# Kernel tuning notes

Hardware: AMD Instinct MI355X
Metric: run time of the kernel (lower is better)

## Reference

```python
import jax, jax.numpy as jnp
import numpy as np

B, S, D, H = 8, 1024, 1024, 16
DK = D // H
EPS = 1e-5

def _layernorm(x, w, b):
    mu = jnp.mean(x, axis=-1, keepdims=True)
    var = jnp.mean((x - mu) ** 2, axis=-1, keepdims=True)
    return (x - mu) * jax.lax.rsqrt(var + EPS) * w + b

def setup_inputs() -> dict:
    key = jax.random.key(0)
    ks = jax.random.split(key, 12)
    x = jax.random.normal(ks[0], (B, S, D), dtype=jnp.float32)
    batch_lengths = jax.random.randint(ks[1], (B,), S // 2, S + 1, dtype=jnp.int32)
    sc = 1.0 / np.sqrt(D)
    Wq = jax.random.normal(ks[2], (H, D, DK), dtype=jnp.float32) * sc
    Wk = jax.random.normal(ks[3], (H, D, DK), dtype=jnp.float32) * sc
    Wv = jax.random.normal(ks[4], (H, D, DK), dtype=jnp.float32) * sc
    fc1_w = jax.random.normal(ks[5], (D, D), dtype=jnp.float32) * sc
    fc1_b = jnp.zeros((D,), dtype=jnp.float32)
    fc2_w = jax.random.normal(ks[6], (D, D), dtype=jnp.float32) * sc
    fc2_b = jnp.zeros((D,), dtype=jnp.float32)
    ln1_w = jnp.ones((D,), dtype=jnp.float32)
    ln1_b = jnp.zeros((D,), dtype=jnp.float32)
    ln2_w = jnp.ones((D,), dtype=jnp.float32)
    ln2_b = jnp.zeros((D,), dtype=jnp.float32)
    return {"x": x, "Wq": Wq, "Wk": Wk, "Wv": Wv, "fc1_w": fc1_w, "fc1_b": fc1_b,
            "fc2_w": fc2_w, "fc2_b": fc2_b, "ln1_w": ln1_w, "ln1_b": ln1_b,
            "ln2_w": ln2_w, "ln2_b": ln2_b, "batch_lengths": batch_lengths, "max_len": S}

def reference(x, Wq, Wk, Wv, fc1_w, fc1_b, fc2_w, fc2_b, ln1_w, ln1_b, ln2_w, ln2_b, batch_lengths, max_len):
    b, s, d = x.shape
    h, _, dk = Wq.shape
    # padding masks: valid positions are t < length
    row = (jnp.arange(s)[None, :] < batch_lengths[:, None]).astype(x.dtype)  # [B,S]
    m = row[:, :, None]                 # [B,S,1], outputMask per-row
    mh = m[:, None]                     # [B,1,S,1]
    # all heads batched: Q,K,V -> [B,H,S,dk], masked like Wq(ctx)*mask etc.
    Q = jnp.einsum('bsd,hde->bhse', x, Wq) * mh
    K = jnp.einsum('bsd,hde->bhse', x, Wk) * mh
    V = jnp.einsum('bsd,hde->bhse', x, Wv) * mh
    energy = jnp.einsum('bhqe,bhke->bhqk', Q, K)
    # attnMask: key columns beyond length -> -inf
    key_valid = row[:, None, None, :] > 0
    energy = jnp.where(key_valid, energy, -jnp.inf)
    score = jax.nn.softmax(energy / jnp.sqrt(jnp.asarray(dk, x.dtype)), axis=-1)
    z = jnp.einsum('bhqk,bhke->bhqe', score, V)           # [B,H,S,dk]
    z = z.transpose(0, 2, 1, 3).reshape(b, s, d) * m      # concat heads, mask
    x1 = _layernorm(x + z, ln1_w, ln1_b)
    ff = jax.nn.relu(x1 @ fc1_w + fc1_b) * m
    ff = (ff @ fc2_w + fc2_b) * m
    return _layernorm(x1 + ff, ln2_w, ln2_b)
```

## Files before the change

### kernel.cpp

```cpp
#include <hip/hip_runtime.h>
#include <math.h>

#define B_ 8
#define S_ 1024
#define D_ 1024
#define H_ 16
#define DK_ 64
#define EPS_ 1e-5f

typedef __bf16 bf16_t;
typedef __bf16 bf16x8 __attribute__((ext_vector_type(8)));
typedef __bf16 bf16x4v __attribute__((ext_vector_type(4)));
typedef float  f32x4  __attribute__((ext_vector_type(4)));

__device__ __forceinline__ void gld16(const void* g, void* l) {
    __builtin_amdgcn_global_load_lds(
        (const __attribute__((address_space(1))) void*)g,
        (__attribute__((address_space(3))) void*)l, 16, 0, 0);
}

__global__ __launch_bounds__(256)
void prep(const float* __restrict__ x,
          const float* __restrict__ Wq, const float* __restrict__ Wk,
          const float* __restrict__ Wv, const float* __restrict__ W1,
          const float* __restrict__ W2, bf16_t* __restrict__ xb,
          bf16_t* __restrict__ WtQKV, bf16_t* __restrict__ Wt1,
          bf16_t* __restrict__ Wt2)
{
    __shared__ float tile[64][65];
    const int tid = threadIdx.x;
    const int z = blockIdx.z;

    if (z >= 5) {
        const int blk = (z - 5) * 256 + blockIdx.y * 16 + blockIdx.x;
        const int i = (blk * 256 + tid) * 4;
        const float4 v = *(const float4*)(x + i);
        bf16x4v o = { (bf16_t)v.x, (bf16_t)v.y, (bf16_t)v.z, (bf16_t)v.w };
        *(bf16x4v*)(xb + i) = o;
        return;
    }

    const int n0 = blockIdx.x * 64, k0 = blockIdx.y * 64;
    const int col = tid & 63, r0 = tid >> 6;
    const float* src = (z == 0) ? Wq : (z == 1) ? Wk : (z == 2) ? Wv
                     : (z == 3) ? W1 : W2;
    #pragma unroll
    for (int i = 0; i < 16; i++) {
        const int row = r0 + i * 4;
        float v;
        if (z < 3)
            v = src[((size_t)(n0 >> 6) << 16) + (size_t)(k0 + row) * 64 + col];
        else
            v = src[(size_t)(k0 + row) * D_ + n0 + col];
        tile[row][col] = v;
    }
    __syncthreads();
    bf16_t* dst = (z < 3) ? (WtQKV + (size_t)z * D_ * D_)
                : (z == 3) ? Wt1 : Wt2;
    #pragma unroll
    for (int i = 0; i < 16; i++) {
        const int nr = r0 + i * 4;
        const int n = n0 + nr, k = k0 + col;
        const size_t pidx = ((size_t)(n >> 4) * (D_ >> 3) + (k >> 3)) * 128
                          + (size_t)(n & 15) * 8 + (k & 7);
        dst[pidx] = (bf16_t)tile[col][nr];
    }
}

template<int EPI, typename OUT>
__global__ __launch_bounds__(256, 2)
void gemm_bp(const bf16_t* __restrict__ A, const bf16_t* __restrict__ Bp,
             const float* __restrict__ bias, const int* __restrict__ lens,
             OUT* __restrict__ C, int M, int N, int K)
{
    __shared__ __align__(16) bf16_t As[2][128 * 64];

    const int tid  = threadIdx.x;
    const int lane = tid & 63;
    const int w    = tid >> 6;
    const int quad = lane >> 4, l16 = lane & 15;
    const int wm = w & 1, wn = w >> 1;
    const int sw8 = l16 & 7;

    const int nwg  = gridDim.x * gridDim.y;
    const int orig = blockIdx.y * gridDim.x + blockIdx.x;
    const int swz  = (orig & 7) * (nwg >> 3) + (orig >> 3);
    const int bn = (swz % gridDim.x) * 128;
    const int bm = (swz / gridDim.x) * 128;

    const int rS  = tid >> 3;
    const int cS  = ((tid & 7) ^ (rS & 7)) << 3;
    const int dOf = w * 1024;

    const size_t ntStride = (size_t)(K >> 3) * 128;
    const bf16_t* Bw = Bp + ((size_t)(bn >> 4) + (size_t)wn * 4) * ntStride
                          + (size_t)quad * 128 + (size_t)l16 * 8;

    f32x4 acc[4][4];
    #pragma unroll
    for (int i = 0; i < 4; i++)
        #pragma unroll
        for (int j = 0; j < 4; j++)
            #pragma unroll
            for (int r = 0; r < 4; r++) acc[i][j][r] = 0.f;

#define SA(b_, kt_) { \
    _Pragma("unroll") \
    for (int s_ = 0; s_ < 4; s_++) \
        gld16(A + (size_t)(bm + s_ * 32 + rS) * K + (kt_) * 64 + cS, \
              (char*)As[b_] + s_ * 4096 + dOf); }
#define LB(dst_, kt_) { \
    _Pragma("unroll") \
    for (int j_ = 0; j_ < 4; j_++) \
        _Pragma("unroll") \
        for (int kh_ = 0; kh_ < 2; kh_++) \
            dst_[j_][kh_] = *(const bf16x8*)(Bw + (size_t)j_ * ntStride \
                                             + ((kt_) * 8 + kh_ * 4) * 128); }
#define KSTEP(cb_, nb_, BC_, BX_, t_) { \
    const int ktn_ = ((t_) + 1 < NKT) ? (t_) + 1 : (t_); \
    SA(nb_, ktn_); \
    LB(BX_, ktn_); \
    __builtin_amdgcn_sched_barrier(0); \
    const bf16_t* Ac = As[cb_]; \
    _Pragma("unroll") \
    for (int kh_ = 0; kh_ < 2; kh_++) { \
        bf16x8 a_[4]; \
        _Pragma("unroll") \
        for (int i_ = 0; i_ < 4; i_++) \
            a_[i_] = *(const bf16x8*)&Ac[(wm * 64 + i_ * 16 + l16) * 64 \
                                         + (((kh_ * 4 + quad) ^ sw8) << 3)]; \
        _Pragma("unroll") \
        for (int i_ = 0; i_ < 4; i_++) \
            _Pragma("unroll") \
            for (int j_ = 0; j_ < 4; j_++) \
                acc[i_][j_] = __builtin_amdgcn_mfma_f32_16x16x32_bf16( \
                    a_[i_], BC_[j_][kh_], acc[i_][j_], 0, 0, 0); \
    } \
    __builtin_amdgcn_sched_barrier(0); \
    asm volatile("s_waitcnt vmcnt(8)" ::: "memory"); \
    __builtin_amdgcn_s_barrier(); }

    const int NKT = K >> 6;

    bf16x8 bA[4][2], bB[4][2];
    SA(0, 0);
    LB(bA, 0);
    asm volatile("s_waitcnt vmcnt(8)" ::: "memory");
    __builtin_amdgcn_s_barrier();

    for (int t = 0; t < NKT; t += 2) {
        KSTEP(0, 1, bA, bB, t);
        KSTEP(1, 0, bB, bA, t + 1);
    }

#undef SA
#undef LB
#undef KSTEP

    #pragma unroll
    for (int i = 0; i < 4; i++) {
        #pragma unroll
        for (int r = 0; r < 4; r++) {
            const int m = bm + wm * 64 + i * 16 + quad * 4 + r;
            float keep = 1.f;
            if (EPI != 0) {
                const int s = m & (S_ - 1);
                const int bb = m >> 10;
                keep = (s < lens[bb]) ? 1.f : 0.f;
            }
            #pragma unroll
            for (int j = 0; j < 4; j++) {
                const int n = bn + wn * 64 + j * 16 + l16;
                float v = acc[i][j][r];
                if (EPI != 0) {
                    v += bias[n];
                    if (EPI == 1) v = fmaxf(v, 0.f);
                    v *= keep;
                }
                C[(size_t)m * N + n] = (OUT)v;
            }
        }
    }
}

__global__ __launch_bounds__(512, 4)
void attn_mfma(const bf16_t* __restrict__ QKV, const int* __restrict__ lens,
               bf16_t* __restrict__ Z)
{
    __shared__ __align__(16) bf16_t Ks[2][64][64];
    __shared__ __align__(16) bf16_t Vt[2][64][72];
    __shared__ __align__(16) bf16_t Ps[128][72];

    const int tid  = threadIdx.x;
    const int lane = tid & 63;
    const int w    = tid >> 6;
    const int quad = lane >> 4;
    const int l16  = lane & 15;
    const int id   = blockIdx.x;
    const int b    = id & 7;
    const int h    = (id >> 3) & 15;
    const int qt   = id >> 7;
    const int len  = lens[b];
    const int qbase = qt * 128;
    const bf16_t* Qp = QKV + (size_t)b * S_ * 3072 + (size_t)h * 64;
    const bf16_t* Kp = Qp + 1024;
    const bf16_t* Vp = Qp + 2048;
    const size_t zbase = (size_t)b * S_ * D_ + (size_t)h * 64;

    if (qbase >= len) {
        const int r = tid >> 2, c0 = (tid & 3) * 16;
        bf16_t* zp = Z + zbase + (size_t)(qbase + r) * D_ + c0;
        uint4 zz = {0u, 0u, 0u, 0u};
        *(uint4*)zp = zz;
        *(uint4*)(zp + 8) = zz;
        return;
    }

    const int qrow = qbase + w * 16 + l16;
    const bf16x8 bq0 = *(const bf16x8*)(Qp + (size_t)qrow * 3072 + quad * 8);
    const bf16x8 bq1 = *(const bf16x8*)(Qp + (size_t)qrow * 3072 + 32 + quad * 8);

    const int kr = tid >> 3;
    const int kc = ((tid & 7) ^ (kr & 7)) << 3;

    const int vr  = tid >> 3;
    const int cg8 = tid & 7;
    const int vc0 = cg8 * 8;
    const int vp  = vr ^ ((cg8 >> 1) << 4);

    f32x4 o[4];
    #pragma unroll
    for (int dm = 0; dm < 4; dm++)
        #pragma unroll
        for (int r = 0; r < 4; r++) o[dm][r] = 0.f;
    float l_q = 0.f;

    const int ntiles = (len + 63) >> 6;

    gld16(Kp + (size_t)kr * 3072 + kc, (char*)&Ks[0][0][0] + w * 1024);
    bf16x8 vcur = *(const bf16x8*)(Vp + (size_t)vr * 3072 + vc0);
    __syncthreads();

    for (int t = 0; t < ntiles; t++) {
        const int k0 = t * 64;
        const int cb = t & 1, nb = (t + 1) & 1;
        const int kn0 = (t + 1 < ntiles ? t + 1 : t) * 64;

        gld16(Kp + (size_t)(kn0 + kr) * 3072 + kc, (char*)&Ks[nb][0][0] + w * 1024);
        const bf16x8 vn = *(const bf16x8*)(Vp + (size_t)(kn0 + vr) * 3072 + vc0);
        __builtin_amdgcn_sched_barrier(0);

        #pragma unroll
        for (int kt = 0; kt < 4; kt++) {
            const int r = kt * 16 + l16;
            const bf16x8 ak0 = *(const bf16x8*)&Ks[cb][r][(quad ^ (l16 & 7)) << 3];
            const bf16x8 ak1 = *(const bf16x8*)&Ks[cb][r][((4 + quad) ^ (l16 & 7)) << 3];
            f32x4 z4 = {0.f, 0.f, 0.f, 0.f};
            z4 = __builtin_amdgcn_mfma_f32_16x16x32_bf16(ak0, bq0, z4, 0, 0, 0);
            const f32x4 sfv = __builtin_amdgcn_mfma_f32_16x16x32_bf16(ak1, bq1, z4, 0, 0, 0);
            bf16x4v pk;
            #pragma unroll
            for (int r2 = 0; r2 < 4; r2++) {
                const int key = k0 + kt * 16 + quad * 4 + r2;
                float p = __expf(sfv[r2] * 0.125f);
                p = (key < len) ? p : 0.f;
                l_q += p;
                pk[r2] = (bf16_t)p;
            }
            *(bf16x4v*)&Ps[w * 16 + l16][kt * 16 + quad * 4] = pk;
        }

        #pragma unroll
        for (int i = 0; i < 8; i++) Vt[cb][vc0 + i][vp] = vcur[i];
        vcur = vn;
        __syncthreads();

        const bf16x8 bp0 = *(const bf16x8*)&Ps[w * 16 + l16][quad * 8];
        const bf16x8 bp1 = *(const bf16x8*)&Ps[w * 16 + l16][32 + quad * 8];
        #pragma unroll
        for (int dm = 0; dm < 4; dm++) {
            const bf16x8 av0 = *(const bf16x8*)&Vt[cb][dm * 16 + l16][(quad * 8) ^ (dm * 16)];
            const bf16x8 av1 = *(const bf16x8*)&Vt[cb][dm * 16 + l16][(32 + quad * 8) ^ (dm * 16)];
            o[dm] = __builtin_amdgcn_mfma_f32_16x16x32_bf16(av0, bp0, o[dm], 0, 0, 0);
            o[dm] = __builtin_amdgcn_mfma_f32_16x16x32_bf16(av1, bp1, o[dm], 0, 0, 0);
        }
    }

    l_q += __shfl_xor(l_q, 16);
    l_q += __shfl_xor(l_q, 32);
    const int qg = qbase + w * 16 + l16;
    const float inv = (qg < len) ? 1.f / l_q : 0.f;
    bf16_t* zrow = Z + zbase + (size_t)qg * D_;
    #pragma unroll
    for (int dm = 0; dm < 4; dm++) {
        bf16x4v st;
        #pragma unroll
        for (int r = 0; r < 4; r++) st[r] = (bf16_t)(o[dm][r] * inv);
        *(bf16x4v*)(zrow + dm * 16 + quad * 4) = st;
    }
}

__device__ __forceinline__ void ln_core(float vx, float vy, float vz, float vw,
                                        int tid, float& mean, float& rstd)
{
    __shared__ float red[8];
    float s = vx + vy + vz + vw;
    #pragma unroll
    for (int off = 32; off; off >>= 1) s += __shfl_xor(s, off, 64);
    const int wv = tid >> 6, lane = tid & 63;
    if (lane == 0) red[wv] = s;
    __syncthreads();
    mean = (red[0] + red[1] + red[2] + red[3]) * (1.f / D_);
    const float dx = vx - mean, dy = vy - mean, dz = vz - mean, dw = vw - mean;
    float s2 = dx * dx + dy * dy + dz * dz + dw * dw;
    #pragma unroll
    for (int off = 32; off; off >>= 1) s2 += __shfl_xor(s2, off, 64);
    if (lane == 0) red[4 + wv] = s2;
    __syncthreads();
    rstd = rsqrtf((red[4] + red[5] + red[6] + red[7]) * (1.f / D_) + EPS_);
}

__global__ __launch_bounds__(256)
void add_ln1(const float* __restrict__ X, const bf16_t* __restrict__ Y,
             const float* __restrict__ g, const float* __restrict__ beta,
             bf16_t* __restrict__ out)
{
    const int row = blockIdx.x, tid = threadIdx.x;
    const float4 xv = ((const float4*)(X + (size_t)row * D_))[tid];
    const bf16x4v yv = *(const bf16x4v*)(Y + (size_t)row * D_ + tid * 4);
    const float vx = xv.x + (float)yv[0], vy = xv.y + (float)yv[1];
    const float vz = xv.z + (float)yv[2], vw = xv.w + (float)yv[3];
    float mean, rstd;
    ln_core(vx, vy, vz, vw, tid, mean, rstd);
    const float4 gv = ((const float4*)g)[tid];
    const float4 bv = ((const float4*)beta)[tid];
    bf16x4v o;
    o[0] = (bf16_t)((vx - mean) * rstd * gv.x + bv.x);
    o[1] = (bf16_t)((vy - mean) * rstd * gv.y + bv.y);
    o[2] = (bf16_t)((vz - mean) * rstd * gv.z + bv.z);
    o[3] = (bf16_t)((vw - mean) * rstd * gv.w + bv.w);
    *(bf16x4v*)(out + (size_t)row * D_ + tid * 4) = o;
}

__global__ __launch_bounds__(256)
void add_ln2(const bf16_t* __restrict__ X, const float* __restrict__ Y,
             const float* __restrict__ g, const float* __restrict__ beta,
             float* __restrict__ out)
{
    const int row = blockIdx.x, tid = threadIdx.x;
    const bf16x4v xv = *(const bf16x4v*)(X + (size_t)row * D_ + tid * 4);
    const float4 yv = ((const float4*)(Y + (size_t)row * D_))[tid];
    const float vx = (float)xv[0] + yv.x, vy = (float)xv[1] + yv.y;
    const float vz = (float)xv[2] + yv.z, vw = (float)xv[3] + yv.w;
    float mean, rstd;
    ln_core(vx, vy, vz, vw, tid, mean, rstd);
    const float4 gv = ((const float4*)g)[tid];
    const float4 bv = ((const float4*)beta)[tid];
    float4 o;
    o.x = (vx - mean) * rstd * gv.x + bv.x;
    o.y = (vy - mean) * rstd * gv.y + bv.y;
    o.z = (vz - mean) * rstd * gv.z + bv.z;
    o.w = (vw - mean) * rstd * gv.w + bv.w;
    ((float4*)(out + (size_t)row * D_))[tid] = o;
}

extern "C" void kernel_launch(void* const* d_in, const int* in_sizes, int n_in,
                              void* d_out, int out_size, void* d_ws, size_t ws_size,
                              hipStream_t stream)
{
    const float* x    = (const float*)d_in[0];
    const float* Wq   = (const float*)d_in[1];
    const float* Wk   = (const float*)d_in[2];
    const float* Wv   = (const float*)d_in[3];
    const float* fc1w = (const float*)d_in[4];
    const float* fc1b = (const float*)d_in[5];
    const float* fc2w = (const float*)d_in[6];
    const float* fc2b = (const float*)d_in[7];
    const float* ln1w = (const float*)d_in[8];
    const float* ln1b = (const float*)d_in[9];
    const float* ln2w = (const float*)d_in[10];
    const float* ln2b = (const float*)d_in[11];
    const int*   lens = (const int*)d_in[12];
    float* out = (float*)d_out;

    char* ws = (char*)d_ws;
    const size_t MB = 1024 * 1024;
    bf16_t* QKVb  = (bf16_t*)(ws);
    bf16_t* Zb    = (bf16_t*)(ws + 48 * MB);
    bf16_t* X1b   = (bf16_t*)(ws + 80 * MB);
    bf16_t* xb    = (bf16_t*)(ws + 96 * MB);
    bf16_t* H1b   = (bf16_t*)(ws + 96 * MB);
    float*  FF    = (float*)(ws + 48 * MB);
    bf16_t* WtQKV = (bf16_t*)(ws + 112 * MB);
    bf16_t* Wt1   = (bf16_t*)(ws + 118 * MB);
    bf16_t* Wt2   = (bf16_t*)(ws + 120 * MB);

    const int M = B_ * S_;

    prep<<<dim3(16, 16, 37), 256, 0, stream>>>(x, Wq, Wk, Wv, fc1w, fc2w,
                                               xb, WtQKV, Wt1, Wt2);

    gemm_bp<0, bf16_t><<<dim3(3072 / 128, M / 128), 256, 0, stream>>>(
        xb, WtQKV, nullptr, nullptr, QKVb, M, 3072, D_);

    attn_mfma<<<dim3(1024), 512, 0, stream>>>(QKVb, lens, Zb);

    add_ln1<<<M, 256, 0, stream>>>(x, Zb, ln1w, ln1b, X1b);

    gemm_bp<1, bf16_t><<<dim3(D_ / 128, M / 128), 256, 0, stream>>>(
        X1b, Wt1, fc1b, lens, H1b, M, D_, D_);
    gemm_bp<2, float><<<dim3(D_ / 128, M / 128), 256, 0, stream>>>(
        H1b, Wt2, fc2b, lens, FF, M, D_, D_);

    add_ln2<<<M, 256, 0, stream>>>(X1b, FF, ln2w, ln2b, out);
}
```

Baseline: 305.4 us.

## Write V transposed from QKV GEMM epilogue and async-load it in attention

Result: no change. 304.4 us (-0.3%).

```diff
diff --git a/kernel.cpp b/kernel.cpp
--- a/kernel.cpp
+++ b/kernel.cpp
@@ -71,7 +71,8 @@
 __global__ __launch_bounds__(256, 2)
 void gemm_bp(const bf16_t* __restrict__ A, const bf16_t* __restrict__ Bp,
              const float* __restrict__ bias, const int* __restrict__ lens,
-             OUT* __restrict__ C, int M, int N, int K)
+             OUT* __restrict__ C, bf16_t* __restrict__ VTout,
+             int M, int N, int NC, int K)
 {
     __shared__ __align__(16) bf16_t As[2][128 * 64];
 
@@ -157,6 +158,22 @@
 #undef LB
 #undef KSTEP
 
+    if (EPI == 0 && bn >= 2048) {
+        #pragma unroll
+        for (int i = 0; i < 4; i++) {
+            const int m0 = bm + wm * 64 + i * 16 + quad * 4;
+            const int bb = m0 >> 10, s0 = m0 & 1023;
+            #pragma unroll
+            for (int j = 0; j < 4; j++) {
+                const int n = bn + wn * 64 + j * 16 + l16;
+                bf16x4v vv;
+                #pragma unroll
+                for (int r = 0; r < 4; r++) vv[r] = (bf16_t)acc[i][j][r];
+                *(bf16x4v*)(VTout + ((size_t)bb * 1024 + (n - 2048)) * 1024 + s0) = vv;
+            }
+        }
+        return;
+    }
     #pragma unroll
     for (int i = 0; i < 4; i++) {
         #pragma unroll
@@ -177,18 +194,18 @@
                     if (EPI == 1) v = fmaxf(v, 0.f);
                     v *= keep;
                 }
-                C[(size_t)m * N + n] = (OUT)v;
+                C[(size_t)m * NC + n] = (OUT)v;
             }
         }
     }
 }
 
-__global__ __launch_bounds__(512, 4)
-void attn_mfma(const bf16_t* __restrict__ QKV, const int* __restrict__ lens,
-               bf16_t* __restrict__ Z)
+__global__ __launch_bounds__(512, 6)
+void attn_mfma(const bf16_t* __restrict__ QK, const bf16_t* __restrict__ VT,
+               const int* __restrict__ lens, bf16_t* __restrict__ Z)
 {
     __shared__ __align__(16) bf16_t Ks[2][64][64];
-    __shared__ __align__(16) bf16_t Vt[2][64][72];
+    __shared__ __align__(16) bf16_t Vs[2][64][64];
     __shared__ __align__(16) bf16_t Ps[128][72];
 
     const int tid  = threadIdx.x;
@@ -202,9 +219,9 @@
     const int qt   = id >> 7;
     const int len  = lens[b];
     const int qbase = qt * 128;
-    const bf16_t* Qp = QKV + (size_t)b * S_ * 3072 + (size_t)h * 64;
-    const bf16_t* Kp = Qp + 1024;
-    const bf16_t* Vp = Qp + 2048;
+    const bf16_t* Qp  = QK + (size_t)b * S_ * 2048 + (size_t)h * 64;
+    const bf16_t* Kp  = Qp + 1024;
+    const bf16_t* Vtp = VT + ((size_t)b * 16 + h) * 64 * 1024;
     const size_t zbase = (size_t)b * S_ * D_ + (size_t)h * 64;
 
     if (qbase >= len) {
@@ -217,16 +234,11 @@
     }
 
     const int qrow = qbase + w * 16 + l16;
-    const bf16x8 bq0 = *(const bf16x8*)(Qp + (size_t)qrow * 3072 + quad * 8);
-    const bf16x8 bq1 = *(const bf16x8*)(Qp + (size_t)qrow * 3072 + 32 + quad * 8);
-
-    const int kr = tid >> 3;
-    const int kc = ((tid & 7) ^ (kr & 7)) << 3;
-
-    const int vr  = tid >> 3;
-    const int cg8 = tid & 7;
-    const int vc0 = cg8 * 8;
-    const int vp  = vr ^ ((cg8 >> 1) << 4);
+    const bf16x8 bq0 = *(const bf16x8*)(Qp + (size_t)qrow * 2048 + quad * 8);
+    const bf16x8 bq1 = *(const bf16x8*)(Qp + (size_t)qrow * 2048 + 32 + quad * 8);
+
+    const int sr = tid >> 3;
+    const int sc = ((tid & 7) ^ (sr & 7)) << 3;
 
     f32x4 o[4];
     #pragma unroll
@@ -237,8 +249,8 @@
 
     const int ntiles = (len + 63) >> 6;
 
-    gld16(Kp + (size_t)kr * 3072 + kc, (char*)&Ks[0][0][0] + w * 1024);
-    bf16x8 vcur = *(const bf16x8*)(Vp + (size_t)vr * 3072 + vc0);
+    gld16(Kp  + (size_t)sr * 2048 + sc, (char*)&Ks[0][0][0] + w * 1024);
+    gld16(Vtp + (size_t)sr * 1024 + sc, (char*)&Vs[0][0][0] + w * 1024);
     __syncthreads();
 
     for (int t = 0; t < ntiles; t++) {
@@ -246,8 +258,8 @@
         const int cb = t & 1, nb = (t + 1) & 1;
         const int kn0 = (t + 1 < ntiles ? t + 1 : t) * 64;
 
-        gld16(Kp + (size_t)(kn0 + kr) * 3072 + kc, (char*)&Ks[nb][0][0] + w * 1024);
-        const bf16x8 vn = *(const bf16x8*)(Vp + (size_t)(kn0 + vr) * 3072 + vc0);
+        gld16(Kp  + (size_t)(kn0 + sr) * 2048 + sc, (char*)&Ks[nb][0][0] + w * 1024);
+        gld16(Vtp + (size_t)sr * 1024 + kn0 + sc,   (char*)&Vs[nb][0][0] + w * 1024);
         __builtin_amdgcn_sched_barrier(0);
 
         #pragma unroll
@@ -270,20 +282,22 @@
             *(bf16x4v*)&Ps[w * 16 + l16][kt * 16 + quad * 4] = pk;
         }
 
-        #pragma unroll
-        for (int i = 0; i < 8; i++) Vt[cb][vc0 + i][vp] = vcur[i];
-        vcur = vn;
         __syncthreads();
 
         const bf16x8 bp0 = *(const bf16x8*)&Ps[w * 16 + l16][quad * 8];
         const bf16x8 bp1 = *(const bf16x8*)&Ps[w * 16 + l16][32 + quad * 8];
         #pragma unroll
         for (int dm = 0; dm < 4; dm++) {
-            const bf16x8 av0 = *(const bf16x8*)&Vt[cb][dm * 16 + l16][(quad * 8) ^ (dm * 16)];
-            const bf16x8 av1 = *(const bf16x8*)&Vt[cb][dm * 16 + l16][(32 + quad * 8) ^ (dm * 16)];
+            const int vr = dm * 16 + l16;
+            const bf16x8 av0 = *(const bf16x8*)&Vs[cb][vr][(quad ^ (l16 & 7)) << 3];
+            const bf16x8 av1 = *(const bf16x8*)&Vs[cb][vr][((4 + quad) ^ (l16 & 7)) << 3];
             o[dm] = __builtin_amdgcn_mfma_f32_16x16x32_bf16(av0, bp0, o[dm], 0, 0, 0);
             o[dm] = __builtin_amdgcn_mfma_f32_16x16x32_bf16(av1, bp1, o[dm], 0, 0, 0);
         }
+
+        __builtin_amdgcn_sched_barrier(0);
+        __builtin_amdgcn_s_barrier();
+        __builtin_amdgcn_sched_barrier(0);
     }
 
     l_q += __shfl_xor(l_q, 16);
@@ -385,7 +399,8 @@
 
     char* ws = (char*)d_ws;
     const size_t MB = 1024 * 1024;
-    bf16_t* QKVb  = (bf16_t*)(ws);
+    bf16_t* QKb   = (bf16_t*)(ws);
+    bf16_t* VTb   = (bf16_t*)(ws + 32 * MB);
     bf16_t* Zb    = (bf16_t*)(ws + 48 * MB);
     bf16_t* X1b   = (bf16_t*)(ws + 80 * MB);
     bf16_t* xb    = (bf16_t*)(ws + 96 * MB);
@@ -401,16 +416,16 @@
                                                xb, WtQKV, Wt1, Wt2);
 
     gemm_bp<0, bf16_t><<<dim3(3072 / 128, M / 128), 256, 0, stream>>>(
-        xb, WtQKV, nullptr, nullptr, QKVb, M, 3072, D_);
-
-    attn_mfma<<<dim3(1024), 512, 0, stream>>>(QKVb, lens, Zb);
+        xb, WtQKV, nullptr, nullptr, QKb, VTb, M, 3072, 2048, D_);
+
+    attn_mfma<<<dim3(1024), 512, 0, stream>>>(QKb, VTb, lens, Zb);
 
     add_ln1<<<M, 256, 0, stream>>>(x, Zb, ln1w, ln1b, X1b);
 
     gemm_bp<1, bf16_t><<<dim3(D_ / 128, M / 128), 256, 0, stream>>>(
-        X1b, Wt1, fc1b, lens, H1b, M, D_, D_);
+        X1b, Wt1, fc1b, lens, H1b, nullptr, M, D_, D_, D_);
     gemm_bp<2, float><<<dim3(D_ / 128, M / 128), 256, 0, stream>>>(
-        H1b, Wt2, fc2b, lens, FF, M, D_, D_);
+        H1b, Wt2, fc2b, lens, FF, nullptr, M, D_, D_, D_);
 
     add_ln2<<<M, 256, 0, stream>>>(X1b, FF, ln2w, ln2b, out);
 }
```
